# Kernel optimization log

Hardware: AMD Instinct MI355X
Metric: run time of the kernel (lower is better)

The kernel has to match this reference:

```python
import jax, jax.numpy as jnp
import numpy as np

N = 8192  # nv + nh, bias=False


def setup_inputs() -> dict:
    key = jax.random.key(0)
    k1, k2, k3, k4 = jax.random.split(key, 4)
    w = jax.random.normal(k1, (N, N), dtype=jnp.float32) * 0.01  # learned [n,n] coupling matrix
    initial_state = jax.random.randint(k2, (N,), 0, 2).astype(jnp.float32)  # binary unit states
    clamping_degree = jnp.zeros((N,), dtype=jnp.float32)  # 0 => unit is free to update
    T = jnp.float32(1.0)  # temperature
    perm = jax.random.permutation(k3, N).astype(jnp.int32)  # torch.randperm(self.n)
    rand_u = jax.random.uniform(k4, (N,), dtype=jnp.float32)  # torch.rand(1) per unit
    return {"w": w, "initial_state": initial_state, "clamping_degree": clamping_degree,
            "T": T, "perm": perm, "rand_u": rand_u}


def reference(w, initial_state, clamping_degree, T, perm, rand_u):
    # Sequential Gibbs sweep: for each j in perm, if unclamped,
    # p = sigmoid(w[j]@state / T); state[j] = 1 if u <= p else 0.
    inactive = jnp.float32(0.0)

    def step(state, ju):
        j, u = ju
        sum_input = jnp.dot(w[j], state)          # per-unit dot product against current state
        p = jax.nn.sigmoid(sum_input / T)          # 1/(1+exp(-x/T))
        new_val = jnp.where(u <= p, jnp.float32(1.0), inactive)
        upd = jnp.where(clamping_degree[j] == 0, new_val, state[j])
        return state.at[j].set(upd), None

    final_state, _ = jax.lax.scan(step, initial_state, (perm, rand_u))
    return final_state
```

## Files before the change

kernel.cpp:

```cpp
#include <hip/hip_runtime.h>
#include <math.h>


#define NN 8192
#define BB 512
#define NBLK 16
#define SUB 64
#define NSUB 8
#define NWG 256
#define NWORK 255
#define TPB 512
#define MAXR 3

typedef unsigned int u32;

__global__ void k_init(u32* flags, int n) {
  int i = blockIdx.x * blockDim.x + threadIdx.x;
  for (; i < n; i += gridDim.x * blockDim.x) flags[i] = 0;
}

__device__ __forceinline__ u32 ld_rlx(const u32* p) {
  return __hip_atomic_load(p, __ATOMIC_RELAXED, __HIP_MEMORY_SCOPE_AGENT);
}
__device__ __forceinline__ u32 ld_acq(const u32* p) {
  return __hip_atomic_load(p, __ATOMIC_ACQUIRE, __HIP_MEMORY_SCOPE_AGENT);
}
__device__ __forceinline__ void st_rlx(u32* p, u32 v) {
  __hip_atomic_store(p, v, __ATOMIC_RELAXED, __HIP_MEMORY_SCOPE_AGENT);
}
__device__ __forceinline__ float ldf_rlx(const float* p) {
  return __hip_atomic_load(p, __ATOMIC_RELAXED, __HIP_MEMORY_SCOPE_AGENT);
}

__global__ __launch_bounds__(TPB) void k_gibbs(
    const float* __restrict__ w, const float* __restrict__ init,
    const float* __restrict__ clampv, const float* __restrict__ Tp,
    const int* __restrict__ perm, const float* __restrict__ urand,
    float* __restrict__ dout, double* __restrict__ S,
    float* __restrict__ delG, float* __restrict__ tileD,
    u32* subFlag, u32* ack) {
  __shared__ float stateL[NN];
  __shared__ double sumsL[BB], thrL[BB];
  __shared__ float d1L[BB], d0L[BB], delL[BB], oldL[BB];
  __shared__ int uL[BB];
  __shared__ double redL[TPB / 64][MAXR];
  const int wg = blockIdx.x, tid = threadIdx.x;
  const int wv = tid >> 6, lane = tid & 63;

  if (wg == 0) {
    double T = (double)Tp[0];
    for (int b = 0; b < NBLK; ++b) {
      int pos = b * BB + tid;
      int unit = perm[pos];
      double uu = (double)urand[pos];
      thrL[tid] = T * log(uu / (1.0 - uu));
      float old = init[unit];
      bool cl = (clampv[unit] != 0.0f);
      d1L[tid] = cl ? 0.0f : (1.0f - old);
      d0L[tid] = cl ? 0.0f : (0.0f - old);
      oldL[tid] = old;
      uL[tid] = unit;
      {
        const u32* slots = ack + (size_t)b * NWORK;
        for (;;) {
          int ok = 1;
          if (tid < NWORK) ok = (ld_rlx(&slots[tid]) != 0u);
          if (__syncthreads_and(ok)) break;
          __builtin_amdgcn_s_sleep(2);
        }
        if (tid == 0) (void)ld_acq(&slots[0]);
        __syncthreads();
      }
      sumsL[tid] = S[(size_t)b * BB + tid];
      __syncthreads();
      const float* tb = tileD + (size_t)b * BB * BB;

      for (int t8 = 0; t8 < NSUB; ++t8) {
        float m[SUB];
        if (tid < SUB) {
          const float4* mr = (const float4*)(tb + (size_t)(t8 * SUB + tid) * BB + t8 * SUB);
#pragma unroll
          for (int j = 0; j < SUB / 4; ++j) {
            float4 v = mr[j];
            m[4*j] = v.x; m[4*j+1] = v.y; m[4*j+2] = v.z; m[4*j+3] = v.w;
          }
        } else if (t8 > 0) {
          int t = tid - SUB, g = t >> 2, sb = t & 3;
          if (g < SUB) {
            int row = t8 * SUB + g;
            int c0 = (t8 - 1) * SUB + sb * 16;
            const float4* mr2 = (const float4*)(tb + (size_t)row * BB + c0);
            double p = 0.0;
#pragma unroll
            for (int j = 0; j < 4; ++j) {
              float4 v = mr2[j];
              p += (double)(v.x * delL[c0+4*j])   + (double)(v.y * delL[c0+4*j+1]) +
                   (double)(v.z * delL[c0+4*j+2]) + (double)(v.w * delL[c0+4*j+3]);
            }
            p += __shfl_down(p, 2, 4);
            p += __shfl_down(p, 1, 4);
            if (sb == 0) sumsL[row] += p;
          }
        }
        __syncthreads();
        if (tid < SUB) {
          int row = t8 * SUB + tid;
          double sum = sumsL[row], th = thrL[row];
          float dd1 = d1L[row], dd0 = d0L[row];
          float mydel = 0.0f;
          __builtin_amdgcn_s_setprio(3);
#pragma unroll
          for (int s = 0; s < SUB; ++s) {
            float down = (sum >= th) ? dd1 : dd0;
            float sd = __uint_as_float(__builtin_amdgcn_readlane(__float_as_uint(down), s));
            if (s == tid) mydel = down;
            sum += (double)(m[s] * sd);
          }
          __builtin_amdgcn_s_setprio(0);
          delL[row] = mydel;
          if (b + 1 < NBLK) {
            delG[b * BB + row] = mydel;
            __threadfence();
            if (tid == 0) st_rlx(&subFlag[b * NSUB + t8], 1u);
          }
        } else if (t8 > 0) {
          for (int r = (t8 + 1) * SUB + (tid - SUB); r < BB; r += (TPB - SUB)) {
            int c0 = (t8 - 1) * SUB;
            const float4* mr3 = (const float4*)(tb + (size_t)r * BB + c0);
            double acc = sumsL[r];
#pragma unroll
            for (int j = 0; j < SUB / 4; ++j) {
              float4 v = mr3[j];
              acc += (double)(v.x * delL[c0+4*j])   + (double)(v.y * delL[c0+4*j+1]) +
                     (double)(v.z * delL[c0+4*j+2]) + (double)(v.w * delL[c0+4*j+3]);
            }
            sumsL[r] = acc;
          }
        }
        __syncthreads();
      }
      dout[uL[tid]] = oldL[tid] + delL[tid];
    }
  } else {
    const int iw = wg - 1;
    const int r0 = (iw * BB) / NWORK, r1 = ((iw + 1) * BB) / NWORK;
    const int cnt = r1 - r0;
    for (int i = tid; i < NN; i += TPB) stateL[i] = init[i];
    __syncthreads();

    for (int p = 0; p < NBLK; ++p) {
      int pc = perm[p * BB + tid];
      float g[NSUB];
      float* tbp = tileD + (size_t)p * BB * BB;

      for (int ri = 0; ri < cnt; ++ri) {
        int unit = perm[p * BB + r0 + ri];
        const float* wrow = w + (size_t)unit * NN;
        const float4* wr4 = (const float4*)wrow;
        const float4* st4 = (const float4*)stateL;
        double acc = 0.0;
#pragma unroll
        for (int k = 0; k < NN / (4 * TPB); ++k) {
          float4 a = wr4[tid + k * TPB];
          float4 s = st4[tid + k * TPB];
          acc += (double)(a.x * s.x) + (double)(a.y * s.y) +
                 (double)(a.z * s.z) + (double)(a.w * s.w);
        }
        for (int o = 32; o > 0; o >>= 1) acc += __shfl_down(acc, o, 64);
        if (lane == 0) redL[wv][ri] = acc;
        tbp[(size_t)(r0 + ri) * BB + tid] = wrow[pc];
        if (p > 0 && wv == ri) {
#pragma unroll
          for (int t8 = 0; t8 < NSUB; ++t8)
            g[t8] = wrow[perm[(p - 1) * BB + t8 * SUB + lane]];
        }
      }
      __syncthreads();
      double Sr = 0.0;
      if (wv < cnt) {
#pragma unroll
        for (int k = 0; k < TPB / 64; ++k) Sr += redL[k][wv];
      }
      if (p > 0) {
        double crr = 0.0;
        for (int t8 = 0; t8 < NSUB; ++t8) {
          const u32* f = &subFlag[(p - 1) * NSUB + t8];
          if (tid == 0) {
            while (ld_rlx(f) == 0u) __builtin_amdgcn_s_sleep(2);
          }
          __syncthreads();
          float dl = ldf_rlx(&delG[(p - 1) * BB + t8 * SUB + lane]);
          if (wv < cnt) crr += (double)(g[t8] * dl);
          if (tid < SUB) stateL[perm[(p - 1) * BB + t8 * SUB + tid]] += dl;
        }
        for (int o = 32; o > 0; o >>= 1) crr += __shfl_down(crr, o, 64);
        Sr += crr;
        __syncthreads();
      }
      if (wv < cnt && lane == 0) S[(size_t)p * BB + r0 + wv] = Sr;
      __syncthreads();
      if (tid == 0) {
        __threadfence();
        st_rlx(&ack[(size_t)p * NWORK + iw], 1u);
      }
      __syncthreads();
    }
  }
}

extern "C" void kernel_launch(void* const* d_in, const int* in_sizes, int n_in,
                              void* d_out, int out_size, void* d_ws, size_t ws_size,
                              hipStream_t stream) {
  const float* w      = (const float*)d_in[0];
  const float* init   = (const float*)d_in[1];
  const float* clampv = (const float*)d_in[2];
  const float* Tp     = (const float*)d_in[3];
  const int*   perm   = (const int*)d_in[4];
  const float* urand  = (const float*)d_in[5];
  float* dout = (float*)d_out;

  double* S    = (double*)d_ws;
  float* delG  = (float*)(S + NN);
  float* tileD = delG + NN;
  u32* subFlag = (u32*)(tileD + (size_t)NBLK * BB * BB);
  u32* ack     = subFlag + NBLK * NSUB;

  int nflags = NBLK * NSUB + NBLK * NWORK;
  k_init<<<8, 256, 0, stream>>>(subFlag, nflags);

  void* args[] = {(void*)&w, (void*)&init, (void*)&clampv, (void*)&Tp,
                  (void*)&perm, (void*)&urand, (void*)&dout,
                  (void*)&S, (void*)&delG, (void*)&tileD,
                  (void*)&subFlag, (void*)&ack};
  hipLaunchCooperativeKernel((const void*)k_gibbs, dim3(NWG), dim3(TPB),
                             args, 0, stream);
}
```

Before: 575.1 us.

## Double-buffer diagonal tiles, prefetch next-subblock rows, and drop fences in Gibbs handshake

The serial chain in workgroup 0 now double-buffers the diagonal 64x64 sub-tile, loading the next one while the current chain runs. The next sub-block's off-diagonal rows are prefetched into registers by the upper threads so the correction can start immediately. Publication of delta values moves to relaxed atomic stores, with flags signalled one iteration later instead of after a threadfence. Worker-side fences, an acquire load and a barrier are removed and sleep intervals are shortened. The aim is to cut latency on the critical sequential path, at the risk of weaker memory ordering, since relaxed atomics alone are relied on for visibility.

```diff
diff --git a/kernel.cpp b/kernel.cpp
--- a/kernel.cpp
+++ b/kernel.cpp
@@ -22,15 +22,48 @@
 __device__ __forceinline__ u32 ld_rlx(const u32* p) {
   return __hip_atomic_load(p, __ATOMIC_RELAXED, __HIP_MEMORY_SCOPE_AGENT);
 }
-__device__ __forceinline__ u32 ld_acq(const u32* p) {
-  return __hip_atomic_load(p, __ATOMIC_ACQUIRE, __HIP_MEMORY_SCOPE_AGENT);
-}
 __device__ __forceinline__ void st_rlx(u32* p, u32 v) {
   __hip_atomic_store(p, v, __ATOMIC_RELAXED, __HIP_MEMORY_SCOPE_AGENT);
 }
 __device__ __forceinline__ float ldf_rlx(const float* p) {
   return __hip_atomic_load(p, __ATOMIC_RELAXED, __HIP_MEMORY_SCOPE_AGENT);
 }
+__device__ __forceinline__ void stf_rlx(float* p, float v) {
+  __hip_atomic_store(p, v, __ATOMIC_RELAXED, __HIP_MEMORY_SCOPE_AGENT);
+}
+__device__ __forceinline__ double ldd_rlx(const double* p) {
+  return __hip_atomic_load(p, __ATOMIC_RELAXED, __HIP_MEMORY_SCOPE_AGENT);
+}
+__device__ __forceinline__ void std_rlx(double* p, double v) {
+  __hip_atomic_store(p, v, __ATOMIC_RELAXED, __HIP_MEMORY_SCOPE_AGENT);
+}
+
+#define LOADM(MARR, T8N) do {                                                  \
+  const float4* mr_ = (const float4*)(tb + (size_t)((T8N) * SUB + tid) * BB + (T8N) * SUB); \
+  _Pragma("unroll")                                                            \
+  for (int j_ = 0; j_ < SUB / 4; ++j_) {                                       \
+    float4 v_ = mr_[j_];                                                       \
+    MARR[4*j_] = v_.x; MARR[4*j_+1] = v_.y;                                    \
+    MARR[4*j_+2] = v_.z; MARR[4*j_+3] = v_.w; }                                \
+} while (0)
+
+#define CHAIN(MARR, T8C) do {                                                  \
+  int row_ = (T8C) * SUB + tid;                                                \
+  double sum_ = sumsL[row_], th_ = thrL[row_];                                 \
+  float dd1_ = d1L[row_], dd0_ = d0L[row_];                                    \
+  float mydel_ = 0.0f;                                                         \
+  __builtin_amdgcn_s_setprio(3);                                               \
+  _Pragma("unroll")                                                            \
+  for (int s_ = 0; s_ < SUB; ++s_) {                                           \
+    float down_ = (sum_ >= th_) ? dd1_ : dd0_;                                 \
+    float sd_ = __uint_as_float(                                               \
+        __builtin_amdgcn_readlane(__float_as_uint(down_), s_));                \
+    if (s_ == tid) mydel_ = down_;                                             \
+    sum_ += (double)(MARR[s_] * sd_); }                                        \
+  __builtin_amdgcn_s_setprio(0);                                               \
+  delL[row_] = mydel_;                                                         \
+  if (pub) stf_rlx(&delG[b * BB + row_], mydel_);                              \
+} while (0)
 
 __global__ __launch_bounds__(TPB) void k_gibbs(
     const float* __restrict__ w, const float* __restrict__ init,
@@ -50,6 +83,7 @@
   if (wg == 0) {
     double T = (double)Tp[0];
     for (int b = 0; b < NBLK; ++b) {
+      const bool pub = (b + 1 < NBLK);
       int pos = b * BB + tid;
       int unit = perm[pos];
       double uu = (double)urand[pos];
@@ -66,79 +100,68 @@
           int ok = 1;
           if (tid < NWORK) ok = (ld_rlx(&slots[tid]) != 0u);
           if (__syncthreads_and(ok)) break;
-          __builtin_amdgcn_s_sleep(2);
-        }
-        if (tid == 0) (void)ld_acq(&slots[0]);
-        __syncthreads();
-      }
-      sumsL[tid] = S[(size_t)b * BB + tid];
+          __builtin_amdgcn_s_sleep(1);
+        }
+      }
+      sumsL[tid] = ldd_rlx(&S[(size_t)b * BB + tid]);
       __syncthreads();
       const float* tb = tileD + (size_t)b * BB * BB;
+      float mA[SUB], mB[SUB];
+      float4 nv0, nv1, nv2, nv3;
+      if (tid < SUB) LOADM(mA, 0);
 
       for (int t8 = 0; t8 < NSUB; ++t8) {
-        float m[SUB];
-        if (tid < SUB) {
-          const float4* mr = (const float4*)(tb + (size_t)(t8 * SUB + tid) * BB + t8 * SUB);
-#pragma unroll
-          for (int j = 0; j < SUB / 4; ++j) {
-            float4 v = mr[j];
-            m[4*j] = v.x; m[4*j+1] = v.y; m[4*j+2] = v.z; m[4*j+3] = v.w;
-          }
-        } else if (t8 > 0) {
-          int t = tid - SUB, g = t >> 2, sb = t & 3;
-          if (g < SUB) {
-            int row = t8 * SUB + g;
-            int c0 = (t8 - 1) * SUB + sb * 16;
-            const float4* mr2 = (const float4*)(tb + (size_t)row * BB + c0);
-            double p = 0.0;
-#pragma unroll
-            for (int j = 0; j < 4; ++j) {
-              float4 v = mr2[j];
-              p += (double)(v.x * delL[c0+4*j])   + (double)(v.y * delL[c0+4*j+1]) +
-                   (double)(v.z * delL[c0+4*j+2]) + (double)(v.w * delL[c0+4*j+3]);
-            }
-            p += __shfl_down(p, 2, 4);
-            p += __shfl_down(p, 1, 4);
-            if (sb == 0) sumsL[row] += p;
+        if (t8 > 0) {
+          if (pub && tid == 0) st_rlx(&subFlag[b * NSUB + (t8 - 1)], 1u);
+          if (tid >= 256) {
+            int t = tid - 256;
+            int rrow = t8 * SUB + (t >> 2);
+            int q = t & 3;
+            int c0 = (t8 - 1) * SUB + q * 16;
+            double p_ =
+                (double)(nv0.x * delL[c0])    + (double)(nv0.y * delL[c0+1]) +
+                (double)(nv0.z * delL[c0+2])  + (double)(nv0.w * delL[c0+3]) +
+                (double)(nv1.x * delL[c0+4])  + (double)(nv1.y * delL[c0+5]) +
+                (double)(nv1.z * delL[c0+6])  + (double)(nv1.w * delL[c0+7]);
+            p_ +=
+                (double)(nv2.x * delL[c0+8])  + (double)(nv2.y * delL[c0+9]) +
+                (double)(nv2.z * delL[c0+10]) + (double)(nv2.w * delL[c0+11]) +
+                (double)(nv3.x * delL[c0+12]) + (double)(nv3.y * delL[c0+13]) +
+                (double)(nv3.z * delL[c0+14]) + (double)(nv3.w * delL[c0+15]);
+            p_ += __shfl_down(p_, 2, 4);
+            p_ += __shfl_down(p_, 1, 4);
+            if (q == 0) sumsL[rrow] += p_;
           }
         }
         __syncthreads();
         if (tid < SUB) {
-          int row = t8 * SUB + tid;
-          double sum = sumsL[row], th = thrL[row];
-          float dd1 = d1L[row], dd0 = d0L[row];
-          float mydel = 0.0f;
-          __builtin_amdgcn_s_setprio(3);
-#pragma unroll
-          for (int s = 0; s < SUB; ++s) {
-            float down = (sum >= th) ? dd1 : dd0;
-            float sd = __uint_as_float(__builtin_amdgcn_readlane(__float_as_uint(down), s));
-            if (s == tid) mydel = down;
-            sum += (double)(m[s] * sd);
-          }
-          __builtin_amdgcn_s_setprio(0);
-          delL[row] = mydel;
-          if (b + 1 < NBLK) {
-            delG[b * BB + row] = mydel;
-            __threadfence();
-            if (tid == 0) st_rlx(&subFlag[b * NSUB + t8], 1u);
-          }
-        } else if (t8 > 0) {
-          for (int r = (t8 + 1) * SUB + (tid - SUB); r < BB; r += (TPB - SUB)) {
-            int c0 = (t8 - 1) * SUB;
-            const float4* mr3 = (const float4*)(tb + (size_t)r * BB + c0);
-            double acc = sumsL[r];
-#pragma unroll
-            for (int j = 0; j < SUB / 4; ++j) {
-              float4 v = mr3[j];
-              acc += (double)(v.x * delL[c0+4*j])   + (double)(v.y * delL[c0+4*j+1]) +
-                     (double)(v.z * delL[c0+4*j+2]) + (double)(v.w * delL[c0+4*j+3]);
+          if (t8 & 1) { if (t8 < NSUB - 1) LOADM(mA, t8 + 1); CHAIN(mB, t8); }
+          else        { if (t8 < NSUB - 1) LOADM(mB, t8 + 1); CHAIN(mA, t8); }
+        } else {
+          if (t8 < NSUB - 1 && tid >= 256) {
+            int t = tid - 256;
+            const float4* pr = (const float4*)(
+                tb + (size_t)((t8 + 1) * SUB + (t >> 2)) * BB + t8 * SUB + (t & 3) * 16);
+            nv0 = pr[0]; nv1 = pr[1]; nv2 = pr[2]; nv3 = pr[3];
+          }
+          if (t8 > 0) {
+            for (int r = (t8 + 1) * SUB + (tid - SUB); r < BB; r += (TPB - SUB)) {
+              int c0 = (t8 - 1) * SUB;
+              const float4* mr3 = (const float4*)(tb + (size_t)r * BB + c0);
+              double acc = sumsL[r];
+#pragma unroll
+              for (int j = 0; j < SUB / 4; ++j) {
+                float4 v = mr3[j];
+                acc += (double)(v.x * delL[c0+4*j])   + (double)(v.y * delL[c0+4*j+1]) +
+                       (double)(v.z * delL[c0+4*j+2]) + (double)(v.w * delL[c0+4*j+3]);
+              }
+              sumsL[r] = acc;
             }
-            sumsL[r] = acc;
           }
         }
         __syncthreads();
       }
+      if (pub && tid == 0) st_rlx(&subFlag[b * NSUB + (NSUB - 1)], 1u);
       dout[uL[tid]] = oldL[tid] + delL[tid];
     }
   } else {
@@ -168,7 +191,7 @@
         }
         for (int o = 32; o > 0; o >>= 1) acc += __shfl_down(acc, o, 64);
         if (lane == 0) redL[wv][ri] = acc;
-        tbp[(size_t)(r0 + ri) * BB + tid] = wrow[pc];
+        stf_rlx(&tbp[(size_t)(r0 + ri) * BB + tid], wrow[pc]);
         if (p > 0 && wv == ri) {
 #pragma unroll
           for (int t8 = 0; t8 < NSUB; ++t8)
@@ -186,7 +209,7 @@
         for (int t8 = 0; t8 < NSUB; ++t8) {
           const u32* f = &subFlag[(p - 1) * NSUB + t8];
           if (tid == 0) {
-            while (ld_rlx(f) == 0u) __builtin_amdgcn_s_sleep(2);
+            while (ld_rlx(f) == 0u) __builtin_amdgcn_s_sleep(1);
           }
           __syncthreads();
           float dl = ldf_rlx(&delG[(p - 1) * BB + t8 * SUB + lane]);
@@ -195,15 +218,10 @@
         }
         for (int o = 32; o > 0; o >>= 1) crr += __shfl_down(crr, o, 64);
         Sr += crr;
-        __syncthreads();
-      }
-      if (wv < cnt && lane == 0) S[(size_t)p * BB + r0 + wv] = Sr;
+      }
+      if (wv < cnt && lane == 0) std_rlx(&S[(size_t)p * BB + r0 + wv], Sr);
       __syncthreads();
-      if (tid == 0) {
-        __threadfence();
-        st_rlx(&ack[(size_t)p * NWORK + iw], 1u);
-      }
-      __syncthreads();
+      if (tid == 0) st_rlx(&ack[(size_t)p * NWORK + iw], 1u);
     }
   }
 }
```

After: 508.6 us. 1.13x faster.
